# Kernel optimization log

Measured on AMD Instinct MI355X. Metric: run time of the kernel, lower is better.

The kernel has to match this reference:

```python
import jax, jax.numpy as jnp
import numpy as np

HEAD = 4

def setup_inputs() -> dict:
    key = jax.random.key(0)
    ks = jax.random.split(key, 6)
    n_nodes = 100000
    n_edges = 1600000
    latdim = 128
    embeds = jax.random.normal(ks[0], (n_nodes, latdim), dtype=jnp.float32)
    qTrans = jax.random.normal(ks[1], (latdim, latdim), dtype=jnp.float32) * (1.0 / np.sqrt(latdim))
    kTrans = jax.random.normal(ks[2], (latdim, latdim), dtype=jnp.float32) * (1.0 / np.sqrt(latdim))
    vTrans = jax.random.normal(ks[3], (latdim, latdim), dtype=jnp.float32) * (1.0 / np.sqrt(latdim))
    rows = jax.random.randint(ks[4], (n_edges,), 0, n_nodes, dtype=jnp.int64) if jax.config.jax_enable_x64 else jax.random.randint(ks[4], (n_edges,), 0, n_nodes, dtype=jnp.int32)
    cols = jax.random.randint(ks[5], (n_edges,), 0, n_nodes, dtype=rows.dtype)
    return {"embeds": embeds, "qTrans": qTrans, "kTrans": kTrans, "vTrans": vTrans,
            "rows": rows, "cols": cols, "n_nodes": n_nodes}


def reference(embeds, qTrans, kTrans, vTrans, rows, cols, n_nodes):
    latdim = embeds.shape[1]
    dh = latdim // HEAD  # per-head dim
    # Gather endpoint embeddings per edge: [E, latdim]
    rowEmbeds = embeds[rows]
    colEmbeds = embeds[cols]
    # Per-edge QKV projections reshaped to [E, H, dh]
    q = (rowEmbeds @ qTrans).reshape(-1, HEAD, dh)
    k = (colEmbeds @ kTrans).reshape(-1, HEAD, dh)
    v = (colEmbeds @ vTrans).reshape(-1, HEAD, dh)
    # Per-edge, per-head attention logits
    att = jnp.einsum('ehd,ehd->eh', q, k)
    att = jnp.clip(att, -10.0, 10.0)
    expAtt = jnp.exp(att)
    # Segmented softmax normalization over destination nodes (rows)
    attNorm = jax.ops.segment_sum(expAtt, rows, num_segments=n_nodes)[rows]
    att = expAtt / (attNorm + 1e-8)
    # Weight values and scatter-add back to nodes
    resEdges = (att[:, :, None] * v).reshape(-1, latdim)
    resEmbeds = jax.ops.segment_sum(resEdges, rows, num_segments=n_nodes)
    return resEmbeds, att
```

## Files before the change

### kernel.cpp

```cpp
#include <hip/hip_runtime.h>

#define LAT 128
#define CAP 256

__global__ __launch_bounds__(256) void proj_kernel(
    const float* __restrict__ A,
    const float* __restrict__ Wq, const float* __restrict__ Wk, const float* __restrict__ Wv,
    float* __restrict__ Cq, float* __restrict__ Ckv,
    int N)
{
  __shared__ float eL[64][132];
  __shared__ float wL[64][132];
  const int t = threadIdx.x;
  const int n0 = blockIdx.x * 64;
  const int mat = blockIdx.y;
  const float* W = (mat == 0) ? Wq : (mat == 1) ? Wk : Wv;

  #pragma unroll
  for (int it = 0; it < 8; ++it) {
    int flat = (it * 256 + t) * 4;
    int n = flat >> 7, kk = flat & 127;
    float4 v = make_float4(0.f, 0.f, 0.f, 0.f);
    if (n0 + n < N) v = *(const float4*)(A + (size_t)(n0 + n) * LAT + kk);
    *(float4*)&eL[n][kk] = v;
  }

  const int nl = t & 15;
  const int j0 = t >> 4;
  float acc[4][8] = {};

  for (int kt = 0; kt < 2; ++kt) {
    __syncthreads();
    #pragma unroll
    for (int it = 0; it < 8; ++it) {
      int flat = (it * 256 + t) * 4;
      int kk = flat >> 7, c = flat & 127;
      *(float4*)&wL[kk][c] = *(const float4*)(W + (size_t)(kt * 64 + kk) * LAT + c);
    }
    __syncthreads();
    #pragma unroll 2
    for (int kk = 0; kk < 64; kk += 2) {
      float4 wa0 = *(float4*)&wL[kk][j0 * 4];
      float4 wb0 = *(float4*)&wL[kk][64 + j0 * 4];
      float4 wa1 = *(float4*)&wL[kk + 1][j0 * 4];
      float4 wb1 = *(float4*)&wL[kk + 1][64 + j0 * 4];
      #pragma unroll
      for (int i = 0; i < 4; ++i) {
        float2 e = *(float2*)&eL[nl + 16 * i][kt * 64 + kk];
        acc[i][0] += e.x * wa0.x + e.y * wa1.x;
        acc[i][1] += e.x * wa0.y + e.y * wa1.y;
        acc[i][2] += e.x * wa0.z + e.y * wa1.z;
        acc[i][3] += e.x * wa0.w + e.y * wa1.w;
        acc[i][4] += e.x * wb0.x + e.y * wb1.x;
        acc[i][5] += e.x * wb0.y + e.y * wb1.y;
        acc[i][6] += e.x * wb0.z + e.y * wb1.z;
        acc[i][7] += e.x * wb0.w + e.y * wb1.w;
      }
    }
  }

  #pragma unroll
  for (int i = 0; i < 4; ++i) {
    int n = n0 + nl + 16 * i;
    if (n < N) {
      float* C = (mat == 0) ? (Cq + (size_t)n * LAT)
                            : (Ckv + (size_t)n * 256 + (mat == 2 ? 128 : 0));
      *(float4*)(C + j0 * 4)      = make_float4(acc[i][0], acc[i][1], acc[i][2], acc[i][3]);
      *(float4*)(C + 64 + j0 * 4) = make_float4(acc[i][4], acc[i][5], acc[i][6], acc[i][7]);
    }
  }
}

__global__ __launch_bounds__(256) void deg_kernel(const int* __restrict__ rows,
                                                  int* __restrict__ counts, int E) {
  int i = blockIdx.x * 256 + threadIdx.x;
  if (i < E) atomicAdd(&counts[rows[i]], 1);
}

__global__ __launch_bounds__(1024) void scan1_kernel(const int* __restrict__ counts,
                                                     int* __restrict__ starts,
                                                     int* __restrict__ bsums, int N) {
  __shared__ int sh[1024];
  int t = threadIdx.x;
  int i = blockIdx.x * 1024 + t;
  int v = (i < N) ? counts[i] : 0;
  sh[t] = v; __syncthreads();
  for (int off = 1; off < 1024; off <<= 1) {
    int x = (t >= off) ? sh[t - off] : 0;
    __syncthreads();
    sh[t] += x;
    __syncthreads();
  }
  if (i < N) starts[i] = sh[t] - v;
  if (t == 1023) bsums[blockIdx.x] = sh[t];
}

__global__ __launch_bounds__(1024) void scan2_kernel(int* __restrict__ bsums, int nb) {
  __shared__ int sh[1024];
  int t = threadIdx.x;
  int v = (t < nb) ? bsums[t] : 0;
  sh[t] = v; __syncthreads();
  for (int off = 1; off < 1024; off <<= 1) {
    int x = (t >= off) ? sh[t - off] : 0;
    __syncthreads();
    sh[t] += x;
    __syncthreads();
  }
  if (t < nb) bsums[t] = sh[t] - v;
}

__global__ __launch_bounds__(256) void scan3_kernel(int* __restrict__ starts,
                                                    const int* __restrict__ bsums,
                                                    int* __restrict__ cursor, int N) {
  int i = blockIdx.x * 256 + threadIdx.x;
  if (i < N) {
    int s = starts[i] + bsums[i >> 10];
    starts[i] = s;
    cursor[i] = s;
  }
}

__global__ __launch_bounds__(256) void fill_kernel(const int* __restrict__ rows,
                                                   const int* __restrict__ cols,
                                                   int* __restrict__ cursor,
                                                   int* __restrict__ eidx,
                                                   int* __restrict__ ecol, int E) {
  int i = blockIdx.x * 256 + threadIdx.x;
  if (i < E) {
    int p = atomicAdd(&cursor[rows[i]], 1);
    eidx[p] = i;
    ecol[p] = cols[i];
  }
}

__global__ __launch_bounds__(256) void attn_kernel(
    const float* __restrict__ KV,
    const int* __restrict__ starts, const int* __restrict__ counts,
    const int* __restrict__ eidx, const int* __restrict__ ecol,
    float* __restrict__ outRes,
    float* __restrict__ outAtt,
    int N)
{
  __shared__ float eaL[4][CAP][4];
  const int w = threadIdx.x >> 6;
  const int lane = threadIdx.x & 63;
  const int n = blockIdx.x * 4 + w;
  if (n >= N) return;
  const int g = lane & 15;
  const int s = lane >> 4;
  const int start = starts[n];
  const int deg = counts[n];

  const float4 q0 = *(const float4*)(outRes + (size_t)n * LAT + g * 8);
  const float4 q1 = *(const float4*)(outRes + (size_t)n * LAT + g * 8 + 4);

  float denom = 0.f;
  float acc[8] = {};
  for (int base = 0; base < deg; base += 64) {
    int j = base + lane;
    int c_l = 0;
    if (j < deg) c_l = ecol[start + j];
    int m = deg - base; if (m > 64) m = 64;
    int steps = (m + 3) >> 2;
    #pragma unroll 2
    for (int st = 0; st < steps; ++st) {
      int jj = st * 4 + s;
      int c = __shfl(c_l, jj);
      bool valid = (jj < m);
      const float* kv = KV + (size_t)c * 256;
      float4 k0 = *(const float4*)(kv + g * 8);
      float4 k1 = *(const float4*)(kv + g * 8 + 4);
      float4 v0 = *(const float4*)(kv + 128 + g * 8);
      float4 v1 = *(const float4*)(kv + 128 + g * 8 + 4);
      float p = q0.x * k0.x + q0.y * k0.y + q0.z * k0.z + q0.w * k0.w
              + q1.x * k1.x + q1.y * k1.y + q1.z * k1.z + q1.w * k1.w;
      p += __shfl_xor(p, 1);
      p += __shfl_xor(p, 2);
      p = fminf(fmaxf(p, -10.f), 10.f);
      float ea = valid ? __expf(p) : 0.f;
      denom += ea;
      acc[0] += ea * v0.x; acc[1] += ea * v0.y; acc[2] += ea * v0.z; acc[3] += ea * v0.w;
      acc[4] += ea * v1.x; acc[5] += ea * v1.y; acc[6] += ea * v1.z; acc[7] += ea * v1.w;
      int idx = base + jj;
      if (valid && (g & 3) == 0 && idx < CAP) eaL[w][idx][g >> 2] = ea;
    }
  }
  denom += __shfl_xor(denom, 16);
  denom += __shfl_xor(denom, 32);
  #pragma unroll
  for (int i = 0; i < 8; ++i) {
    acc[i] += __shfl_xor(acc[i], 16);
    acc[i] += __shfl_xor(acc[i], 32);
  }
  const float rden = 1.f / (denom + 1e-8f);

  if (lane < 16) {
    float4 r0 = make_float4(acc[0] * rden, acc[1] * rden, acc[2] * rden, acc[3] * rden);
    float4 r1 = make_float4(acc[4] * rden, acc[5] * rden, acc[6] * rden, acc[7] * rden);
    *(float4*)(outRes + (size_t)n * LAT + g * 8) = r0;
    *(float4*)(outRes + (size_t)n * LAT + g * 8 + 4) = r1;
  }

  const float r0 = __shfl(rden, 0);
  const float r1 = __shfl(rden, 4);
  const float r2 = __shfl(rden, 8);
  const float r3 = __shfl(rden, 12);

  int capped = deg < CAP ? deg : CAP;
  for (int j = lane; j < capped; j += 64) {
    int e = eidx[start + j];
    float4 a = *(float4*)&eaL[w][j][0];
    a.x *= r0; a.y *= r1; a.z *= r2; a.w *= r3;
    *(float4*)(outAtt + (size_t)e * 4) = a;
  }

  const float myr = (g >> 2) == 0 ? r0 : (g >> 2) == 1 ? r1 : (g >> 2) == 2 ? r2 : r3;
  for (int base = CAP; base < deg; base += 64) {
    int j = base + lane;
    int c_l = 0, e_l = 0;
    if (j < deg) { c_l = ecol[start + j]; e_l = eidx[start + j]; }
    int m = deg - base; if (m > 64) m = 64;
    int steps = (m + 3) >> 2;
    for (int st = 0; st < steps; ++st) {
      int jj = st * 4 + s;
      int c = __shfl(c_l, jj);
      int e = __shfl(e_l, jj);
      bool valid = (jj < m);
      const float* kv = KV + (size_t)c * 256;
      float4 k0 = *(const float4*)(kv + g * 8);
      float4 k1 = *(const float4*)(kv + g * 8 + 4);
      float p = q0.x * k0.x + q0.y * k0.y + q0.z * k0.z + q0.w * k0.w
              + q1.x * k1.x + q1.y * k1.y + q1.z * k1.z + q1.w * k1.w;
      p += __shfl_xor(p, 1);
      p += __shfl_xor(p, 2);
      p = fminf(fmaxf(p, -10.f), 10.f);
      float av = __expf(p) * myr;
      int lb = lane & 48;
      float4 o;
      o.x = __shfl(av, lb + 0);
      o.y = __shfl(av, lb + 4);
      o.z = __shfl(av, lb + 8);
      o.w = __shfl(av, lb + 12);
      if (valid && g == 0) *(float4*)(outAtt + (size_t)e * 4) = o;
    }
  }
}

extern "C" void kernel_launch(void* const* d_in, const int* in_sizes, int n_in,
                              void* d_out, int out_size, void* d_ws, size_t ws_size,
                              hipStream_t stream) {
  const float* embeds = (const float*)d_in[0];
  const float* qT = (const float*)d_in[1];
  const float* kT = (const float*)d_in[2];
  const float* vT = (const float*)d_in[3];
  const int* rows = (const int*)d_in[4];
  const int* cols = (const int*)d_in[5];

  if (in_sizes[1] != LAT * LAT) return;
  const int N = in_sizes[0] / LAT;
  const int E = in_sizes[4];

  float* outRes = (float*)d_out;
  float* outAtt = outRes + (size_t)N * LAT;

  char* w = (char*)d_ws;
  size_t need = (size_t)N * 256 * 4 + (size_t)N * 4 * 3 + 1024 * 4 + (size_t)E * 4 * 2;
  if (ws_size < need) return;
  float* KV = (float*)w;      w += (size_t)N * 256 * 4;
  int* counts = (int*)w;      w += (size_t)N * 4;
  int* starts = (int*)w;      w += (size_t)N * 4;
  int* cursor = (int*)w;      w += (size_t)N * 4;
  int* bsums  = (int*)w;      w += 1024 * 4;
  int* eidx   = (int*)w;      w += (size_t)E * 4;
  int* ecol   = (int*)w;      w += (size_t)E * 4;

  hipMemsetAsync(counts, 0, (size_t)N * 4, stream);

  dim3 pg((N + 63) / 64, 3);
  proj_kernel<<<pg, 256, 0, stream>>>(embeds, qT, kT, vT, outRes, KV, N);

  deg_kernel<<<(E + 255) / 256, 256, 0, stream>>>(rows, counts, E);
  int nb = (N + 1023) / 1024;
  scan1_kernel<<<nb, 1024, 0, stream>>>(counts, starts, bsums, N);
  scan2_kernel<<<1, 1024, 0, stream>>>(bsums, nb);
  scan3_kernel<<<(N + 255) / 256, 256, 0, stream>>>(starts, bsums, cursor, N);
  fill_kernel<<<(E + 255) / 256, 256, 0, stream>>>(rows, cols, cursor, eidx, ecol, E);

  attn_kernel<<<(N + 3) / 4, 256, 0, stream>>>(KV, starts, counts, eidx, ecol,
                                               outRes, outAtt, N);
}
```

Measured before the change: 695.7 us.

## Pack edge arrays, widen per-lane head slices, shrink projection LDS tiles

The edge index and column arrays are packed into one int2 array, so the fill and attention kernels do a single 8-byte access per edge. The attention kernel now covers 8 edges per step, with each lane owning 16 dims, and prefetches the next edge's packed entry instead of loading a batch and broadcasting with shuffles. The projection kernel streams both embeddings and weights in 32-wide K chunks, which cuts LDS use and should raise occupancy. CAP drops to 64, so nodes with more edges fall back to a slow scalar per-lane recompute for the overflow attention outputs.

Result: slower. 719.1 us (+3.4%).

```diff
diff --git a/kernel.cpp b/kernel.cpp
--- a/kernel.cpp
+++ b/kernel.cpp
@@ -1,7 +1,7 @@
 #include <hip/hip_runtime.h>
 
 #define LAT 128
-#define CAP 256
+#define CAP 64
 
 __global__ __launch_bounds__(256) void proj_kernel(
     const float* __restrict__ A,
@@ -9,44 +9,43 @@
     float* __restrict__ Cq, float* __restrict__ Ckv,
     int N)
 {
-  __shared__ float eL[64][132];
-  __shared__ float wL[64][132];
+  __shared__ float eL[64][36];
+  __shared__ float wL[32][132];
   const int t = threadIdx.x;
   const int n0 = blockIdx.x * 64;
   const int mat = blockIdx.y;
   const float* W = (mat == 0) ? Wq : (mat == 1) ? Wk : Wv;
 
-  #pragma unroll
-  for (int it = 0; it < 8; ++it) {
-    int flat = (it * 256 + t) * 4;
-    int n = flat >> 7, kk = flat & 127;
-    float4 v = make_float4(0.f, 0.f, 0.f, 0.f);
-    if (n0 + n < N) v = *(const float4*)(A + (size_t)(n0 + n) * LAT + kk);
-    *(float4*)&eL[n][kk] = v;
-  }
-
   const int nl = t & 15;
   const int j0 = t >> 4;
   float acc[4][8] = {};
 
-  for (int kt = 0; kt < 2; ++kt) {
+  for (int kt = 0; kt < 4; ++kt) {
     __syncthreads();
     #pragma unroll
-    for (int it = 0; it < 8; ++it) {
+    for (int it = 0; it < 2; ++it) {
+      int flat = (it * 256 + t) * 4;
+      int n = flat >> 5, kk = flat & 31;
+      float4 v = make_float4(0.f, 0.f, 0.f, 0.f);
+      if (n0 + n < N) v = *(const float4*)(A + (size_t)(n0 + n) * LAT + kt * 32 + kk);
+      *(float4*)&eL[n][kk] = v;
+    }
+    #pragma unroll
+    for (int it = 0; it < 4; ++it) {
       int flat = (it * 256 + t) * 4;
       int kk = flat >> 7, c = flat & 127;
-      *(float4*)&wL[kk][c] = *(const float4*)(W + (size_t)(kt * 64 + kk) * LAT + c);
-    }
-    __syncthreads();
-    #pragma unroll 2
-    for (int kk = 0; kk < 64; kk += 2) {
+      *(float4*)&wL[kk][c] = *(const float4*)(W + (size_t)(kt * 32 + kk) * LAT + c);
+    }
+    __syncthreads();
+    #pragma unroll 4
+    for (int kk = 0; kk < 32; kk += 2) {
       float4 wa0 = *(float4*)&wL[kk][j0 * 4];
       float4 wb0 = *(float4*)&wL[kk][64 + j0 * 4];
       float4 wa1 = *(float4*)&wL[kk + 1][j0 * 4];
       float4 wb1 = *(float4*)&wL[kk + 1][64 + j0 * 4];
       #pragma unroll
       for (int i = 0; i < 4; ++i) {
-        float2 e = *(float2*)&eL[nl + 16 * i][kt * 64 + kk];
+        float2 e = *(float2*)&eL[nl + 16 * i][kk];
         acc[i][0] += e.x * wa0.x + e.y * wa1.x;
         acc[i][1] += e.x * wa0.y + e.y * wa1.y;
         acc[i][2] += e.x * wa0.z + e.y * wa1.z;
@@ -123,20 +122,18 @@
 __global__ __launch_bounds__(256) void fill_kernel(const int* __restrict__ rows,
                                                    const int* __restrict__ cols,
                                                    int* __restrict__ cursor,
-                                                   int* __restrict__ eidx,
-                                                   int* __restrict__ ecol, int E) {
+                                                   int2* __restrict__ epack, int E) {
   int i = blockIdx.x * 256 + threadIdx.x;
   if (i < E) {
     int p = atomicAdd(&cursor[rows[i]], 1);
-    eidx[p] = i;
-    ecol[p] = cols[i];
+    epack[p] = make_int2(i, cols[i]);
   }
 }
 
 __global__ __launch_bounds__(256) void attn_kernel(
     const float* __restrict__ KV,
     const int* __restrict__ starts, const int* __restrict__ counts,
-    const int* __restrict__ eidx, const int* __restrict__ ecol,
+    const int2* __restrict__ epack,
     float* __restrict__ outRes,
     float* __restrict__ outAtt,
     int N)
@@ -146,103 +143,103 @@
   const int lane = threadIdx.x & 63;
   const int n = blockIdx.x * 4 + w;
   if (n >= N) return;
-  const int g = lane & 15;
-  const int s = lane >> 4;
+  const int g = lane & 7;
+  const int s = lane >> 3;
   const int start = starts[n];
   const int deg = counts[n];
 
-  const float4 q0 = *(const float4*)(outRes + (size_t)n * LAT + g * 8);
-  const float4 q1 = *(const float4*)(outRes + (size_t)n * LAT + g * 8 + 4);
+  const float* qp = outRes + (size_t)n * LAT + g * 16;
+  const float4 q0 = *(const float4*)(qp + 0);
+  const float4 q1 = *(const float4*)(qp + 4);
+  const float4 q2 = *(const float4*)(qp + 8);
+  const float4 q3 = *(const float4*)(qp + 12);
 
   float denom = 0.f;
-  float acc[8] = {};
-  for (int base = 0; base < deg; base += 64) {
-    int j = base + lane;
-    int c_l = 0;
-    if (j < deg) c_l = ecol[start + j];
-    int m = deg - base; if (m > 64) m = 64;
-    int steps = (m + 3) >> 2;
-    #pragma unroll 2
-    for (int st = 0; st < steps; ++st) {
-      int jj = st * 4 + s;
-      int c = __shfl(c_l, jj);
-      bool valid = (jj < m);
-      const float* kv = KV + (size_t)c * 256;
-      float4 k0 = *(const float4*)(kv + g * 8);
-      float4 k1 = *(const float4*)(kv + g * 8 + 4);
-      float4 v0 = *(const float4*)(kv + 128 + g * 8);
-      float4 v1 = *(const float4*)(kv + 128 + g * 8 + 4);
-      float p = q0.x * k0.x + q0.y * k0.y + q0.z * k0.z + q0.w * k0.w
-              + q1.x * k1.x + q1.y * k1.y + q1.z * k1.z + q1.w * k1.w;
-      p += __shfl_xor(p, 1);
-      p += __shfl_xor(p, 2);
-      p = fminf(fmaxf(p, -10.f), 10.f);
-      float ea = valid ? __expf(p) : 0.f;
-      denom += ea;
-      acc[0] += ea * v0.x; acc[1] += ea * v0.y; acc[2] += ea * v0.z; acc[3] += ea * v0.w;
-      acc[4] += ea * v1.x; acc[5] += ea * v1.y; acc[6] += ea * v1.z; acc[7] += ea * v1.w;
-      int idx = base + jj;
-      if (valid && (g & 3) == 0 && idx < CAP) eaL[w][idx][g >> 2] = ea;
-    }
-  }
+  float acc[16] = {};
+
+  const int steps = (deg + 7) >> 3;
+  int2 ep = make_int2(0, 0);
+  if (deg > 0) ep = epack[start + (s < deg ? s : deg - 1)];
+
+  for (int st = 0; st < steps; ++st) {
+    const int j = st * 8 + s;
+    const bool valid = (j < deg);
+    const int c = ep.y;
+    const int e = ep.x;
+    int jn = j + 8;
+    ep = epack[start + (jn < deg ? jn : deg - 1)];
+
+    const float* kv = KV + (size_t)c * 256 + g * 16;
+    float4 k0 = *(const float4*)(kv + 0);
+    float4 k1 = *(const float4*)(kv + 4);
+    float4 k2 = *(const float4*)(kv + 8);
+    float4 k3 = *(const float4*)(kv + 12);
+    float4 v0 = *(const float4*)(kv + 128);
+    float4 v1 = *(const float4*)(kv + 132);
+    float4 v2 = *(const float4*)(kv + 136);
+    float4 v3 = *(const float4*)(kv + 140);
+
+    float p = q0.x * k0.x + q0.y * k0.y + q0.z * k0.z + q0.w * k0.w
+            + q1.x * k1.x + q1.y * k1.y + q1.z * k1.z + q1.w * k1.w
+            + q2.x * k2.x + q2.y * k2.y + q2.z * k2.z + q2.w * k2.w
+            + q3.x * k3.x + q3.y * k3.y + q3.z * k3.z + q3.w * k3.w;
+    p += __shfl_xor(p, 1);
+    p = fminf(fmaxf(p, -10.f), 10.f);
+    float ea = valid ? __expf(p) : 0.f;
+    denom += ea;
+    acc[0]  += ea * v0.x; acc[1]  += ea * v0.y; acc[2]  += ea * v0.z; acc[3]  += ea * v0.w;
+    acc[4]  += ea * v1.x; acc[5]  += ea * v1.y; acc[6]  += ea * v1.z; acc[7]  += ea * v1.w;
+    acc[8]  += ea * v2.x; acc[9]  += ea * v2.y; acc[10] += ea * v2.z; acc[11] += ea * v2.w;
+    acc[12] += ea * v3.x; acc[13] += ea * v3.y; acc[14] += ea * v3.z; acc[15] += ea * v3.w;
+    if (valid && !(g & 1) && j < CAP) eaL[w][j][g >> 1] = ea;
+  }
+
+  denom += __shfl_xor(denom, 8);
   denom += __shfl_xor(denom, 16);
   denom += __shfl_xor(denom, 32);
   #pragma unroll
-  for (int i = 0; i < 8; ++i) {
+  for (int i = 0; i < 16; ++i) {
+    acc[i] += __shfl_xor(acc[i], 8);
     acc[i] += __shfl_xor(acc[i], 16);
     acc[i] += __shfl_xor(acc[i], 32);
   }
   const float rden = 1.f / (denom + 1e-8f);
 
-  if (lane < 16) {
-    float4 r0 = make_float4(acc[0] * rden, acc[1] * rden, acc[2] * rden, acc[3] * rden);
-    float4 r1 = make_float4(acc[4] * rden, acc[5] * rden, acc[6] * rden, acc[7] * rden);
-    *(float4*)(outRes + (size_t)n * LAT + g * 8) = r0;
-    *(float4*)(outRes + (size_t)n * LAT + g * 8 + 4) = r1;
-  }
-
   const float r0 = __shfl(rden, 0);
-  const float r1 = __shfl(rden, 4);
-  const float r2 = __shfl(rden, 8);
-  const float r3 = __shfl(rden, 12);
-
-  int capped = deg < CAP ? deg : CAP;
+  const float r1 = __shfl(rden, 2);
+  const float r2 = __shfl(rden, 4);
+  const float r3 = __shfl(rden, 6);
+
+  const int capped = deg < CAP ? deg : CAP;
   for (int j = lane; j < capped; j += 64) {
-    int e = eidx[start + j];
+    int e = epack[start + j].x;
     float4 a = *(float4*)&eaL[w][j][0];
     a.x *= r0; a.y *= r1; a.z *= r2; a.w *= r3;
     *(float4*)(outAtt + (size_t)e * 4) = a;
   }
 
-  const float myr = (g >> 2) == 0 ? r0 : (g >> 2) == 1 ? r1 : (g >> 2) == 2 ? r2 : r3;
-  for (int base = CAP; base < deg; base += 64) {
-    int j = base + lane;
-    int c_l = 0, e_l = 0;
-    if (j < deg) { c_l = ecol[start + j]; e_l = eidx[start + j]; }
-    int m = deg - base; if (m > 64) m = 64;
-    int steps = (m + 3) >> 2;
-    for (int st = 0; st < steps; ++st) {
-      int jj = st * 4 + s;
-      int c = __shfl(c_l, jj);
-      int e = __shfl(e_l, jj);
-      bool valid = (jj < m);
-      const float* kv = KV + (size_t)c * 256;
-      float4 k0 = *(const float4*)(kv + g * 8);
-      float4 k1 = *(const float4*)(kv + g * 8 + 4);
-      float p = q0.x * k0.x + q0.y * k0.y + q0.z * k0.z + q0.w * k0.w
-              + q1.x * k1.x + q1.y * k1.y + q1.z * k1.z + q1.w * k1.w;
-      p += __shfl_xor(p, 1);
-      p += __shfl_xor(p, 2);
-      p = fminf(fmaxf(p, -10.f), 10.f);
-      float av = __expf(p) * myr;
-      int lb = lane & 48;
-      float4 o;
-      o.x = __shfl(av, lb + 0);
-      o.y = __shfl(av, lb + 4);
-      o.z = __shfl(av, lb + 8);
-      o.w = __shfl(av, lb + 12);
-      if (valid && g == 0) *(float4*)(outAtt + (size_t)e * 4) = o;
-    }
+  for (int j = CAP + lane; j < deg; j += 64) {
+    int2 epf = epack[start + j];
+    const float* kvp = KV + (size_t)epf.y * 256;
+    const float* qr = outRes + (size_t)n * LAT;
+    float4 o;
+    float* op = (float*)&o;
+    #pragma unroll
+    for (int h = 0; h < 4; ++h) {
+      float d = 0.f;
+      for (int dd = 0; dd < 32; ++dd) d += qr[h * 32 + dd] * kvp[h * 32 + dd];
+      d = fminf(fmaxf(d, -10.f), 10.f);
+      op[h] = __expf(d) * (h == 0 ? r0 : h == 1 ? r1 : h == 2 ? r2 : r3);
+    }
+    *(float4*)(outAtt + (size_t)epf.x * 4) = o;
+  }
+
+  if (lane < 8) {
+    float* rp = outRes + (size_t)n * LAT + g * 16;
+    *(float4*)(rp + 0)  = make_float4(acc[0] * rden,  acc[1] * rden,  acc[2] * rden,  acc[3] * rden);
+    *(float4*)(rp + 4)  = make_float4(acc[4] * rden,  acc[5] * rden,  acc[6] * rden,  acc[7] * rden);
+    *(float4*)(rp + 8)  = make_float4(acc[8] * rden,  acc[9] * rden,  acc[10] * rden, acc[11] * rden);
+    *(float4*)(rp + 12) = make_float4(acc[12] * rden, acc[13] * rden, acc[14] * rden, acc[15] * rden);
   }
 }
 
@@ -264,15 +261,14 @@
   float* outAtt = outRes + (size_t)N * LAT;
 
   char* w = (char*)d_ws;
-  size_t need = (size_t)N * 256 * 4 + (size_t)N * 4 * 3 + 1024 * 4 + (size_t)E * 4 * 2;
+  size_t need = (size_t)N * 256 * 4 + (size_t)N * 4 * 3 + 1024 * 4 + (size_t)E * 8;
   if (ws_size < need) return;
   float* KV = (float*)w;      w += (size_t)N * 256 * 4;
   int* counts = (int*)w;      w += (size_t)N * 4;
   int* starts = (int*)w;      w += (size_t)N * 4;
   int* cursor = (int*)w;      w += (size_t)N * 4;
   int* bsums  = (int*)w;      w += 1024 * 4;
-  int* eidx   = (int*)w;      w += (size_t)E * 4;
-  int* ecol   = (int*)w;      w += (size_t)E * 4;
+  int2* epack = (int2*)w;     w += (size_t)E * 8;
 
   hipMemsetAsync(counts, 0, (size_t)N * 4, stream);
 
@@ -284,8 +280,8 @@
   scan1_kernel<<<nb, 1024, 0, stream>>>(counts, starts, bsums, N);
   scan2_kernel<<<1, 1024, 0, stream>>>(bsums, nb);
   scan3_kernel<<<(N + 255) / 256, 256, 0, stream>>>(starts, bsums, cursor, N);
-  fill_kernel<<<(E + 255) / 256, 256, 0, stream>>>(rows, cols, cursor, eidx, ecol, E);
-
-  attn_kernel<<<(N + 3) / 4, 256, 0, stream>>>(KV, starts, counts, eidx, ecol,
+  fill_kernel<<<(E + 255) / 256, 256, 0, stream>>>(rows, cols, cursor, epack, E);
+
+  attn_kernel<<<(N + 3) / 4, 256, 0, stream>>>(KV, starts, counts, epack,
                                                outRes, outAtt, N);
 }
```
